# Kernel optimization log

Measured on AMD Instinct MI355X. Metric: run time of the kernel, lower is better.

The kernel has to match this reference:

```python
import jax, jax.numpy as jnp
import numpy as np

NV = 10000
NF = 20000
BATCH = 8


def _make_faces(nv, nf):
    # Synthetic closed-ish mesh connectivity: each vertex touches several faces,
    # guaranteeing every diagonal (degree) entry is > 0.
    i = np.arange(nf)
    half = nf // 2
    f0 = i % nv
    f1 = np.where(i < half, (i + 1) % nv, (i + 3) % nv)
    f2 = np.where(i < half, (i + 2) % nv, (i + 5) % nv)
    return np.stack([f0, f1, f2], axis=1).astype(np.int64)


def _build_laplacian(nv, faces):
    # Faithful replication of LaplacianLoss.__init__ (assignment, not accumulation).
    L = np.zeros((nv, nv), dtype=np.float32)
    f0, f1, f2 = faces[:, 0], faces[:, 1], faces[:, 2]
    L[f0, f1] = -1
    L[f1, f0] = -1
    L[f1, f2] = -1
    L[f2, f1] = -1
    L[f2, f0] = -1
    L[f0, f2] = -1
    r = np.arange(nv)
    L[r, r] = -L.sum(1)  # degree on diagonal
    L /= L[r, r][:, None]  # normalize each row by its diagonal
    return L


def setup_inputs() -> dict:
    key = jax.random.key(0)
    kx, kw = jax.random.split(key)
    faces = _make_faces(NV, NF)
    laplacian = jnp.asarray(_build_laplacian(NV, faces))  # [nv, nv]
    x = jax.random.normal(kx, (BATCH, NV, 3), dtype=jnp.float32)
    vertex_weight = jax.random.uniform(kw, (1,), dtype=jnp.float32) + 0.5
    return {"x": x, "laplacian": laplacian, "vertex_weight": vertex_weight}


def reference(x, laplacian, vertex_weight):
    # lx[b, i, k] = sum_j L[i, j] * x[b, j, k]
    lx = jnp.einsum('ij,bjk->bik', laplacian, x)
    lx = lx * vertex_weight
    # torch.norm over dims (1,2) == Frobenius norm per batch element; scaled by nv
    nv = x.shape[1]
    return jnp.sqrt(jnp.sum(lx * lx, axis=(1, 2))) * nv  # [B]
```

## Files before the change

### kernel.cpp

```cpp
#include <hip/hip_runtime.h>
#include <math.h>


#define NVERT 10000
#define TJ 256
#define NTILES 40
#define TPG 10
#define JG 4
#define RPW 4
#define RPB 16
#define NROWG 625
#define GRID1 (NROWG * JG)
#define GRID2 40

__global__ __launch_bounds__(256, 3) void lap_main(
    const float* __restrict__ x, const float* __restrict__ L,
    float* __restrict__ C) {
  __shared__ __align__(16) float smem[6400];

  const int tid  = threadIdx.x;
  const int lane = tid & 63;
  const int wave = tid >> 6;
  const int rg   = blockIdx.x >> 2;
  const int jg   = blockIdx.x & 3;
  const int row0 = rg * RPB + wave * RPW;

  __align__(16) float acc[RPW][24];
#pragma unroll
  for (int r = 0; r < RPW; ++r)
#pragma unroll
    for (int n = 0; n < 24; ++n) acc[r][n] = 0.f;

  const float4* __restrict__ xg = (const float4*)x;

  for (int tt = 0; tt < TPG; ++tt) {
    const int t = jg * TPG + tt;
    const int jcount = (t == NTILES - 1) ? (NVERT - t * TJ) : TJ;
    __syncthreads();

    const int nf4 = (jcount * 3) >> 2;
    if (tid < nf4) {
#pragma unroll
      for (int b = 0; b < 8; ++b)
        ((float4*)smem)[b * 192 + tid] = xg[b * 7500 + t * 192 + tid];
    }
    __syncthreads();

    const int col0 = t * TJ + 4 * lane;
    if (4 * lane < jcount) {
      __align__(16) float Lv[RPW][4];
#pragma unroll
      for (int r = 0; r < RPW; ++r)
        *(float4*)&Lv[r][0] =
            *(const float4*)(L + (long)(row0 + r) * NVERT + col0);

      const float* xs = smem + 12 * lane;
#pragma unroll
      for (int b = 0; b < 8; ++b) {
        __align__(16) float xv[12];
        *(float4*)&xv[0] = *(const float4*)(xs + b * 768);
        *(float4*)&xv[4] = *(const float4*)(xs + b * 768 + 4);
        *(float4*)&xv[8] = *(const float4*)(xs + b * 768 + 8);
#pragma unroll
        for (int r = 0; r < RPW; ++r)
#pragma unroll
          for (int jj = 0; jj < 4; ++jj)
#pragma unroll
            for (int k = 0; k < 3; ++k)
              acc[r][b * 3 + k] += Lv[r][jj] * xv[jj * 3 + k];
      }
    }
  }

  for (int w = 0; w < 4; ++w) {
    __syncthreads();
    if (wave == w) {
#pragma unroll
      for (int r = 0; r < RPW; ++r)
#pragma unroll
        for (int c = 0; c < 6; ++c)
          *(float4*)&smem[lane * 100 + r * 24 + c * 4] = *(float4*)&acc[r][c * 4];
    }
    __syncthreads();
    if (tid < 96) {
      float s = 0.f;
#pragma unroll
      for (int l = 0; l < 64; ++l) s += smem[l * 100 + tid];
      const int row = rg * RPB + w * RPW + tid / 24;
      atomicAdd(&C[row * 24 + (tid % 24)], s);
    }
  }
}

__global__ __launch_bounds__(256) void lap_reduce(
    const float* __restrict__ C, const float* __restrict__ wv,
    float* __restrict__ out, float* __restrict__ Sg, unsigned* __restrict__ ctr) {
  __shared__ float sS[8];
  const int tid = threadIdx.x;
  if (tid < 8) sS[tid] = 0.f;
  __syncthreads();

  const int row = blockIdx.x * 256 + tid;
  float pb[8] = {0.f, 0.f, 0.f, 0.f, 0.f, 0.f, 0.f, 0.f};
  if (row < NVERT) {
    const float* rp = C + (long)row * 24;
#pragma unroll
    for (int b = 0; b < 8; ++b) {
      float s = 0.f;
#pragma unroll
      for (int k = 0; k < 3; ++k) {
        float v = rp[b * 3 + k];
        s += v * v;
      }
      pb[b] = s;
    }
  }
#pragma unroll
  for (int b = 0; b < 8; ++b) atomicAdd(&sS[b], pb[b]);
  __syncthreads();
  if (tid < 8) atomicAdd(&Sg[tid], sS[tid]);
  __syncthreads();

  if (tid == 0) {
    __threadfence();
    unsigned old = atomicAdd(ctr, 1u);
    if (old == (unsigned)(gridDim.x - 1)) {
      __threadfence();
      const float w = wv[0];
#pragma unroll
      for (int b = 0; b < 8; ++b) {
        float s = atomicAdd(&Sg[b], 0.f);
        out[b] = w * sqrtf(s) * (float)NVERT;
      }
    }
  }
}

extern "C" void kernel_launch(void* const* d_in, const int* in_sizes, int n_in,
                              void* d_out, int out_size, void* d_ws, size_t ws_size,
                              hipStream_t stream) {
  const float* x  = (const float*)d_in[0];
  const float* L  = (const float*)d_in[1];
  const float* wv = (const float*)d_in[2];
  float* out = (float*)d_out;

  float* C       = (float*)d_ws;
  float* Sg      = (float*)((char*)d_ws + 960000);
  unsigned* ctr  = (unsigned*)((char*)d_ws + 960032);

  hipMemsetAsync(d_ws, 0, 960064, stream);
  lap_main<<<GRID1, 256, 0, stream>>>(x, L, C);
  lap_reduce<<<GRID2, 256, 0, stream>>>(C, wv, out, Sg, ctr);
}
```

Baseline: 629.7 us.

## Double-buffer x tiles and prefetch L in registers, halve column groups

The main kernel now splits columns into 2 groups of 20 tiles instead of 4 groups of 10, and keeps double-buffered x tiles in shared memory. The next tile's x values and L columns are loaded into registers while the current tile is computed, leaving one barrier per tile instead of two. This is meant to hide global load latency for the dominant L stream and to cut atomic partial-sum traffic. In exchange it roughly doubles shared memory use and adds register pressure from the prefetch buffers, which could lower occupancy under launch_bounds(256,3).

```diff
diff --git a/kernel.cpp b/kernel.cpp
--- a/kernel.cpp
+++ b/kernel.cpp
@@ -4,59 +4,85 @@
 
 #define NVERT 10000
 #define TJ 256
-#define NTILES 40
-#define TPG 10
-#define JG 4
+#define TPJG 20
 #define RPW 4
 #define RPB 16
-#define NROWG 625
-#define GRID1 (NROWG * JG)
+#define NRG 625
+#define GRID1 (NRG * 2)
 #define GRID2 40
 
 __global__ __launch_bounds__(256, 3) void lap_main(
     const float* __restrict__ x, const float* __restrict__ L,
     float* __restrict__ C) {
-  __shared__ __align__(16) float smem[6400];
+  __shared__ __align__(16) float smem[12288];
 
   const int tid  = threadIdx.x;
   const int lane = tid & 63;
   const int wave = tid >> 6;
-  const int rg   = blockIdx.x >> 2;
-  const int jg   = blockIdx.x & 3;
+  const int rg   = blockIdx.x >> 1;
+  const int jg   = blockIdx.x & 1;
   const int row0 = rg * RPB + wave * RPW;
-
-  __align__(16) float acc[RPW][24];
+  const int t0   = jg * TPJG;
+  const int b0   = 2 * wave;
+
+  float acc[RPW][24];
 #pragma unroll
   for (int r = 0; r < RPW; ++r)
 #pragma unroll
     for (int n = 0; n < 24; ++n) acc[r][n] = 0.f;
 
   const float4* __restrict__ xg = (const float4*)x;
-
-  for (int tt = 0; tt < TPG; ++tt) {
-    const int t = jg * TPG + tt;
-    const int jcount = (t == NTILES - 1) ? (NVERT - t * TJ) : TJ;
-    __syncthreads();
-
-    const int nf4 = (jcount * 3) >> 2;
-    if (tid < nf4) {
-#pragma unroll
-      for (int b = 0; b < 8; ++b)
-        ((float4*)smem)[b * 192 + tid] = xg[b * 7500 + t * 192 + tid];
-    }
-    __syncthreads();
-
-    const int col0 = t * TJ + 4 * lane;
-    if (4 * lane < jcount) {
-      __align__(16) float Lv[RPW][4];
-#pragma unroll
-      for (int r = 0; r < RPW; ++r)
-        *(float4*)&Lv[r][0] =
-            *(const float4*)(L + (long)(row0 + r) * NVERT + col0);
-
-      const float* xs = smem + 12 * lane;
-#pragma unroll
-      for (int b = 0; b < 8; ++b) {
+  float4* const smem4 = (float4*)smem;
+
+  const float* Lb[RPW];
+#pragma unroll
+  for (int r = 0; r < RPW; ++r) Lb[r] = L + (long)(row0 + r) * NVERT;
+
+#pragma unroll
+  for (int bb = 0; bb < 2; ++bb) {
+    const int b = b0 + bb;
+#pragma unroll
+    for (int r = 0; r < 3; ++r) {
+      const int idx = r * 64 + lane;
+      smem4[b * 192 + idx] = xg[b * 7500 + t0 * 192 + idx];
+    }
+  }
+  __align__(16) float Lc[RPW][4];
+  {
+    const int c0 = t0 * TJ + 4 * lane;
+#pragma unroll
+    for (int r = 0; r < RPW; ++r) *(float4*)&Lc[r][0] = *(const float4*)(Lb[r] + c0);
+  }
+  __syncthreads();
+
+#pragma unroll 2
+  for (int tt = 0; tt < TPJG; ++tt) {
+    const int q = tt & 1;
+    const int t = t0 + tt;
+    const bool last = (tt == TPJG - 1);
+    const int jc  = (jg == 1 && tt == TPJG - 1) ? 16 : TJ;
+    const int jcn = (jg == 1 && tt == TPJG - 2) ? 16 : TJ;
+    const int nf4 = (jcn * 3) >> 2;
+
+    float4 sv[2][3];
+    if (!last) {
+#pragma unroll
+      for (int bb = 0; bb < 2; ++bb) {
+        const int b = b0 + bb;
+#pragma unroll
+        for (int r = 0; r < 3; ++r) {
+          const int idx = r * 64 + lane;
+          if (idx < nf4) sv[bb][r] = xg[b * 7500 + (t + 1) * 192 + idx];
+        }
+      }
+    }
+
+    const bool act = (4 * lane < jc);
+    const float* xs = smem + q * 6144 + 12 * lane;
+
+    if (act) {
+#pragma unroll
+      for (int b = 0; b < 4; ++b) {
         __align__(16) float xv[12];
         *(float4*)&xv[0] = *(const float4*)(xs + b * 768);
         *(float4*)&xv[4] = *(const float4*)(xs + b * 768 + 4);
@@ -67,9 +93,51 @@
           for (int jj = 0; jj < 4; ++jj)
 #pragma unroll
             for (int k = 0; k < 3; ++k)
-              acc[r][b * 3 + k] += Lv[r][jj] * xv[jj * 3 + k];
-      }
-    }
+              acc[r][b * 3 + k] += Lc[r][jj] * xv[jj * 3 + k];
+      }
+    }
+
+    if (!last) {
+#pragma unroll
+      for (int bb = 0; bb < 2; ++bb) {
+        const int b = b0 + bb;
+#pragma unroll
+        for (int r = 0; r < 3; ++r) {
+          const int idx = r * 64 + lane;
+          if (idx < nf4) smem4[(1 - q) * 1536 + b * 192 + idx] = sv[bb][r];
+        }
+      }
+    }
+
+    __align__(16) float Ln[RPW][4] = {};
+    if (!last && 4 * lane < jcn) {
+      const int cn = (t + 1) * TJ + 4 * lane;
+#pragma unroll
+      for (int r = 0; r < RPW; ++r) *(float4*)&Ln[r][0] = *(const float4*)(Lb[r] + cn);
+    }
+
+    if (act) {
+#pragma unroll
+      for (int b = 4; b < 8; ++b) {
+        __align__(16) float xv[12];
+        *(float4*)&xv[0] = *(const float4*)(xs + b * 768);
+        *(float4*)&xv[4] = *(const float4*)(xs + b * 768 + 4);
+        *(float4*)&xv[8] = *(const float4*)(xs + b * 768 + 8);
+#pragma unroll
+        for (int r = 0; r < RPW; ++r)
+#pragma unroll
+          for (int jj = 0; jj < 4; ++jj)
+#pragma unroll
+            for (int k = 0; k < 3; ++k)
+              acc[r][b * 3 + k] += Lc[r][jj] * xv[jj * 3 + k];
+      }
+    }
+
+    __syncthreads();
+#pragma unroll
+    for (int r = 0; r < RPW; ++r)
+#pragma unroll
+      for (int jj = 0; jj < 4; ++jj) Lc[r][jj] = Ln[r][jj];
   }
 
   for (int w = 0; w < 4; ++w) {
@@ -144,9 +212,9 @@
   const float* wv = (const float*)d_in[2];
   float* out = (float*)d_out;
 
-  float* C       = (float*)d_ws;
-  float* Sg      = (float*)((char*)d_ws + 960000);
-  unsigned* ctr  = (unsigned*)((char*)d_ws + 960032);
+  float* C      = (float*)d_ws;
+  float* Sg     = (float*)((char*)d_ws + 960000);
+  unsigned* ctr = (unsigned*)((char*)d_ws + 960032);
 
   hipMemsetAsync(d_ws, 0, 960064, stream);
   lap_main<<<GRID1, 256, 0, stream>>>(x, L, C);
```

Result: slower. 1.375 ms (+118.3%).
